# Kernel optimization log

Measured on AMD Instinct MI355X. Metric: run time of the kernel, lower is better.

## Reference

```python
import jax, jax.numpy as jnp
import numpy as np

B, S, D, H, HS = 2, 2048, 1024, 16, 64


def setup_inputs() -> dict:
    key = jax.random.key(0)
    ks = jax.random.split(key, 4)
    x = jax.random.normal(ks[0], (B, S, D), dtype=jnp.float32)
    # causal mask: 1.0 where key_pos <= query_pos, else 0.0
    mask = jnp.tril(jnp.ones((S, S), dtype=jnp.float32))
    w_qkv = jax.random.normal(ks[1], (D, 3, H, HS), dtype=jnp.float32) * 0.02
    b_qkv = jnp.zeros((3, H, HS), dtype=jnp.float32)
    w_proj = jax.random.normal(ks[2], (H, HS, D), dtype=jnp.float32) * 0.02
    b_proj = jnp.zeros((D,), dtype=jnp.float32)
    return {"x": x, "mask": mask, "w_qkv": w_qkv, "b_qkv": b_qkv,
            "w_proj": w_proj, "b_proj": b_proj}


def reference(x, mask, w_qkv, b_qkv, w_proj, b_proj):
    # c_attn: [B,S,D] @ [D,3,H,HS] -> [B,S,3,H,HS]
    qkv = jnp.einsum('bsd,dthc->bsthc', x, w_qkv) + b_qkv
    q, k, v = qkv[:, :, 0], qkv[:, :, 1], qkv[:, :, 2]  # [B,S,H,HS]
    scale = jax.lax.rsqrt(float(HS))
    q = q * scale
    # scores over head_size: [B,H,S(query),S(key)]
    scores = jnp.einsum('bqhc,bkhc->bhqk', q, k)
    scores = scores + (1.0 - mask) * -1e9
    weights = jax.nn.softmax(scores, axis=-1).astype(x.dtype)
    # attn_pdrop = 0.0 / inference: dropout is identity
    attn = jnp.einsum('bhqk,bkhc->bqhc', weights, v)  # [B,S,H,HS]
    out = jnp.einsum('bqhc,hcd->bqd', attn, w_proj) + b_proj
    return out
```

## Files before the change

### kernel.cpp

```cpp
#include <hip/hip_runtime.h>
#include <hip/hip_bf16.h>


#define Bb 2
#define Ss 2048
#define Dd 1024
#define Hh 16
#define HSs 64

typedef __bf16 bf16x8 __attribute__((ext_vector_type(8)));
typedef float  f32x4  __attribute__((ext_vector_type(4)));

__device__ __forceinline__ unsigned short f2bf(float f) {
  unsigned int u = __float_as_uint(f);
  unsigned int lsb = (u >> 16) & 1u;
  u += 0x7fffu + lsb;
  return (unsigned short)(u >> 16);
}

__device__ __forceinline__ void async16(const unsigned short* g, unsigned short* l) {
  __builtin_amdgcn_global_load_lds(
      (const __attribute__((address_space(1))) unsigned int*)g,
      (__attribute__((address_space(3))) unsigned int*)l,
      16, 0, 0);
}

__global__ __launch_bounds__(256) void k_cvt_bf16(const float* __restrict__ in,
                                                  unsigned short* __restrict__ out,
                                                  int n) {
  int i = (blockIdx.x * 256 + threadIdx.x) * 4;
  int stride = gridDim.x * 256 * 4;
  for (; i < n; i += stride) {
    float4 v = *reinterpret_cast<const float4*>(in + i);
    ushort4 o;
    o.x = f2bf(v.x); o.y = f2bf(v.y); o.z = f2bf(v.z); o.w = f2bf(v.w);
    *reinterpret_cast<ushort4*>(out + i) = o;
  }
}

__global__ __launch_bounds__(256) void k_transpose_bf16(const float* __restrict__ in,
                                                        unsigned short* __restrict__ out,
                                                        int R, int C) {
  __shared__ float t[32][33];
  int c0 = blockIdx.x * 32, r0 = blockIdx.y * 32;
  int tx = threadIdx.x, ty = threadIdx.y;
  #pragma unroll
  for (int i = 0; i < 32; i += 8)
    t[ty + i][tx] = in[(size_t)(r0 + ty + i) * C + (c0 + tx)];
  __syncthreads();
  #pragma unroll
  for (int i = 0; i < 32; i += 8)
    out[(size_t)(c0 + ty + i) * R + (r0 + tx)] = f2bf(t[tx][ty + i]);
}

__global__ __launch_bounds__(256) void k_gemm_qkv(const unsigned short* __restrict__ A,
                                                  const unsigned short* __restrict__ Bt,
                                                  const float* __restrict__ bias,
                                                  unsigned short* __restrict__ Qg,
                                                  unsigned short* __restrict__ Kg,
                                                  unsigned short* __restrict__ Vt) {
  __shared__ unsigned short As[128 * 64];
  __shared__ unsigned short Bs[128 * 64];
  const int K = 1024;
  int bid = blockIdx.x;
  int swz = (bid % 8) * 96 + bid / 8;
  int tm = swz / 24, tn = swz % 24;
  int m0 = tm * 128, n0 = tn * 128;
  int tid = threadIdx.x;
  int w = tid >> 6, l = tid & 63;
  int lr = l & 15, lg = l >> 4;
  int wm = (w >> 1) * 64, wn = (w & 1) * 64;
  int srow = l >> 3, scol = (l & 7) * 8;

  f32x4 acc[4][4];
  #pragma unroll
  for (int i = 0; i < 4; ++i)
    #pragma unroll
    for (int j = 0; j < 4; ++j)
      acc[i][j] = (f32x4){0.f, 0.f, 0.f, 0.f};

  for (int k0 = 0; k0 < K; k0 += 64) {
    #pragma unroll
    for (int c = 0; c < 4; ++c) {
      int chunk = w * 4 + c;
      int row = chunk * 8 + srow;
      async16(&A[(size_t)(m0 + row) * K + k0 + scol], &As[chunk * 512]);
      async16(&Bt[(size_t)(n0 + row) * K + k0 + scol], &Bs[chunk * 512]);
    }
    __syncthreads();
    #pragma unroll
    for (int kk = 0; kk < 64; kk += 32) {
      bf16x8 af[4], bfr[4];
      #pragma unroll
      for (int mf = 0; mf < 4; ++mf)
        af[mf] = *reinterpret_cast<const bf16x8*>(&As[(wm + mf * 16 + lr) * 64 + kk + lg * 8]);
      #pragma unroll
      for (int nf = 0; nf < 4; ++nf)
        bfr[nf] = *reinterpret_cast<const bf16x8*>(&Bs[(wn + nf * 16 + lr) * 64 + kk + lg * 8]);
      #pragma unroll
      for (int mf = 0; mf < 4; ++mf)
        #pragma unroll
        for (int nf = 0; nf < 4; ++nf)
          acc[mf][nf] = __builtin_amdgcn_mfma_f32_16x16x32_bf16(af[mf], bfr[nf], acc[mf][nf], 0, 0, 0);
    }
    __syncthreads();
  }

  #pragma unroll
  for (int mf = 0; mf < 4; ++mf) {
    #pragma unroll
    for (int nf = 0; nf < 4; ++nf) {
      int n = n0 + wn + nf * 16 + lr;
      int t = n >> 10, r = n & 1023;
      int h = r >> 6, cc = r & 63;
      float bv = bias[n];
      if (t == 2) {
        int m = m0 + wm + mf * 16 + lg * 4;
        int b = m >> 11, s = m & 2047;
        ushort4 pk;
        pk.x = f2bf(acc[mf][nf][0] + bv);
        pk.y = f2bf(acc[mf][nf][1] + bv);
        pk.z = f2bf(acc[mf][nf][2] + bv);
        pk.w = f2bf(acc[mf][nf][3] + bv);
        *reinterpret_cast<ushort4*>(&Vt[((size_t)(b * Hh + h) * HSs + cc) * Ss + s]) = pk;
      } else {
        #pragma unroll
        for (int j = 0; j < 4; ++j) {
          int m = m0 + wm + mf * 16 + lg * 4 + j;
          int b = m >> 11, s = m & 2047;
          size_t idx = ((size_t)(b * Hh + h) * Ss + s) * HSs + cc;
          float v = acc[mf][nf][j] + bv;
          if (t == 0) Qg[idx] = f2bf(v * 0.1803368801111244f);
          else        Kg[idx] = f2bf(v);
        }
      }
    }
  }
}

__global__ __launch_bounds__(512, 4) void k_attn(const unsigned short* __restrict__ Qg,
                                                 const unsigned short* __restrict__ Kg,
                                                 const unsigned short* __restrict__ Vt,
                                                 unsigned short* __restrict__ Ob) {
  __shared__ unsigned short Ks[2][64 * 64];
  __shared__ unsigned short Vs[2][64 * 64];
  __shared__ unsigned short Ps[8][16 * 72];

  int bid = blockIdx.x;
  int pi = bid >> 5, bh = bid & 31;
  int Q = (pi < 8) ? pi : 23 - pi;
  int b = bh >> 4, h = bh & 15;
  int qs0 = Q * 128;

  int tid = threadIdx.x;
  int w = tid >> 6, l = tid & 63;
  int lr = l & 15, lg = l >> 4;
  int qw = qs0 + w * 16;
  int srow = l >> 3, scol = (l & 7) * 8;
  int swcol = scol ^ (srow << 3);
  int row = w * 8 + srow;

  bf16x8 qf[2];
  #pragma unroll
  for (int kx = 0; kx < 2; ++kx)
    qf[kx] = *reinterpret_cast<const bf16x8*>(
        &Qg[((size_t)bh * Ss + qw + lr) * HSs + kx * 32 + lg * 8]);

  f32x4 oacc[4];
  #pragma unroll
  for (int nf = 0; nf < 4; ++nf) oacc[nf] = (f32x4){0.f, 0.f, 0.f, 0.f};
  float mrun[4], lrun[4];
  #pragma unroll
  for (int j = 0; j < 4; ++j) { mrun[j] = -1e30f; lrun[j] = 0.f; }

  int ntiles = 2 * Q + 2;
  async16(&Kg[((size_t)bh * Ss + row) * HSs + swcol], &Ks[0][w * 512]);
  async16(&Vt[((size_t)bh * HSs + row) * Ss + swcol], &Vs[0][w * 512]);
  __syncthreads();

  for (int t = 0; t < ntiles; ++t) {
    int cur = t & 1;
    if (t + 1 < ntiles) {
      async16(&Kg[((size_t)bh * Ss + (t + 1) * 64 + row) * HSs + swcol], &Ks[cur ^ 1][w * 512]);
      async16(&Vt[((size_t)bh * HSs + row) * Ss + (t + 1) * 64 + swcol], &Vs[cur ^ 1][w * 512]);
    }

    if (t * 64 <= qw + 15) {
      f32x4 sacc[4];
      #pragma unroll
      for (int nf = 0; nf < 4; ++nf) sacc[nf] = (f32x4){0.f, 0.f, 0.f, 0.f};
      __builtin_amdgcn_s_setprio(1);
      #pragma unroll
      for (int kx = 0; kx < 2; ++kx) {
        bf16x8 kf[4];
        #pragma unroll
        for (int nf = 0; nf < 4; ++nf)
          kf[nf] = *reinterpret_cast<const bf16x8*>(
              &Ks[cur][(nf * 16 + lr) * 64 + ((kx * 32 + lg * 8) ^ ((lr & 7) << 3))]);
        #pragma unroll
        for (int nf = 0; nf < 4; ++nf)
          sacc[nf] = __builtin_amdgcn_mfma_f32_16x16x32_bf16(qf[kx], kf[nf], sacc[nf], 0, 0, 0);
      }
      __builtin_amdgcn_s_setprio(0);

      if (t * 64 + 63 > qw) {
        #pragma unroll
        for (int nf = 0; nf < 4; ++nf) {
          int kcol = t * 64 + nf * 16 + lr;
          #pragma unroll
          for (int j = 0; j < 4; ++j) {
            int qg2 = qw + lg * 4 + j;
            if (kcol > qg2) sacc[nf][j] = -1e30f;
          }
        }
      }

      float rmax[4];
      #pragma unroll
      for (int j = 0; j < 4; ++j) {
        float rm = fmaxf(fmaxf(sacc[0][j], sacc[1][j]), fmaxf(sacc[2][j], sacc[3][j]));
        #pragma unroll
        for (int d = 1; d < 16; d <<= 1)
          rm = fmaxf(rm, __shfl_xor(rm, d));
        rmax[j] = rm;
      }
      bool need = (rmax[0] > mrun[0] + 8.f) | (rmax[1] > mrun[1] + 8.f) |
                  (rmax[2] > mrun[2] + 8.f) | (rmax[3] > mrun[3] + 8.f);
      if (__any(need)) {
        #pragma unroll
        for (int j = 0; j < 4; ++j) {
          float mnew = fmaxf(mrun[j], rmax[j]);
          float cf = exp2f(mrun[j] - mnew);
          mrun[j] = mnew;
          lrun[j] *= cf;
          #pragma unroll
          for (int nf = 0; nf < 4; ++nf)
            oacc[nf][j] *= cf;
        }
      }
      #pragma unroll
      for (int j = 0; j < 4; ++j) {
        float psum = 0.f;
        #pragma unroll
        for (int nf = 0; nf < 4; ++nf) {
          float pv = exp2f(sacc[nf][j] - mrun[j]);
          sacc[nf][j] = pv;
          psum += pv;
        }
        #pragma unroll
        for (int d = 1; d < 16; d <<= 1)
          psum += __shfl_xor(psum, d);
        lrun[j] += psum;
      }

      #pragma unroll
      for (int nf = 0; nf < 4; ++nf)
        #pragma unroll
        for (int j = 0; j < 4; ++j)
          Ps[w][(lg * 4 + j) * 72 + nf * 16 + lr] = f2bf(sacc[nf][j]);

      __builtin_amdgcn_s_setprio(1);
      #pragma unroll
      for (int kx = 0; kx < 2; ++kx) {
        bf16x8 pf = *reinterpret_cast<const bf16x8*>(&Ps[w][lr * 72 + kx * 32 + lg * 8]);
        bf16x8 vf[4];
        #pragma unroll
        for (int nf = 0; nf < 4; ++nf)
          vf[nf] = *reinterpret_cast<const bf16x8*>(
              &Vs[cur][(nf * 16 + lr) * 64 + ((kx * 32 + lg * 8) ^ ((lr & 7) << 3))]);
        #pragma unroll
        for (int nf = 0; nf < 4; ++nf)
          oacc[nf] = __builtin_amdgcn_mfma_f32_16x16x32_bf16(pf, vf[nf], oacc[nf], 0, 0, 0);
      }
      __builtin_amdgcn_s_setprio(0);
    }
    __syncthreads();
  }

  #pragma unroll
  for (int j = 0; j < 4; ++j) {
    float rinv = 1.0f / lrun[j];
    int s = qw + lg * 4 + j;
    #pragma unroll
    for (int nf = 0; nf < 4; ++nf) {
      int c = nf * 16 + lr;
      Ob[((size_t)(b * Ss + s)) * Dd + h * HSs + c] = f2bf(oacc[nf][j] * rinv);
    }
  }
}

__global__ __launch_bounds__(256) void k_gemm_out(const unsigned short* __restrict__ A,
                                                  const unsigned short* __restrict__ Bt,
                                                  const float* __restrict__ bias,
                                                  float* __restrict__ Out) {
  __shared__ unsigned short As[128 * 64];
  __shared__ unsigned short Bs[128 * 64];
  const int K = 1024;
  int bid = blockIdx.x;
  int swz = (bid % 8) * 32 + bid / 8;
  int tm = swz / 8, tn = swz % 8;
  int m0 = tm * 128, n0 = tn * 128;
  int tid = threadIdx.x;
  int w = tid >> 6, l = tid & 63;
  int lr = l & 15, lg = l >> 4;
  int wm = (w >> 1) * 64, wn = (w & 1) * 64;
  int srow = l >> 3, scol = (l & 7) * 8;

  f32x4 acc[4][4];
  #pragma unroll
  for (int i = 0; i < 4; ++i)
    #pragma unroll
    for (int j = 0; j < 4; ++j)
      acc[i][j] = (f32x4){0.f, 0.f, 0.f, 0.f};

  for (int k0 = 0; k0 < K; k0 += 64) {
    #pragma unroll
    for (int c = 0; c < 4; ++c) {
      int chunk = w * 4 + c;
      int row = chunk * 8 + srow;
      async16(&A[(size_t)(m0 + row) * K + k0 + scol], &As[chunk * 512]);
      async16(&Bt[(size_t)(n0 + row) * K + k0 + scol], &Bs[chunk * 512]);
    }
    __syncthreads();
    #pragma unroll
    for (int kk = 0; kk < 64; kk += 32) {
      bf16x8 af[4], bfr[4];
      #pragma unroll
      for (int mf = 0; mf < 4; ++mf)
        af[mf] = *reinterpret_cast<const bf16x8*>(&As[(wm + mf * 16 + lr) * 64 + kk + lg * 8]);
      #pragma unroll
      for (int nf = 0; nf < 4; ++nf)
        bfr[nf] = *reinterpret_cast<const bf16x8*>(&Bs[(wn + nf * 16 + lr) * 64 + kk + lg * 8]);
      #pragma unroll
      for (int mf = 0; mf < 4; ++mf)
        #pragma unroll
        for (int nf = 0; nf < 4; ++nf)
          acc[mf][nf] = __builtin_amdgcn_mfma_f32_16x16x32_bf16(af[mf], bfr[nf], acc[mf][nf], 0, 0, 0);
    }
    __syncthreads();
  }

  #pragma unroll
  for (int mf = 0; mf < 4; ++mf)
    #pragma unroll
    for (int nf = 0; nf < 4; ++nf) {
      int n = n0 + wn + nf * 16 + lr;
      float bv = bias[n];
      #pragma unroll
      for (int j = 0; j < 4; ++j) {
        int m = m0 + wm + mf * 16 + lg * 4 + j;
        Out[(size_t)m * 1024 + n] = acc[mf][nf][j] + bv;
      }
    }
}

extern "C" void kernel_launch(void* const* d_in, const int* in_sizes, int n_in,
                              void* d_out, int out_size, void* d_ws, size_t ws_size,
                              hipStream_t stream) {
  (void)in_sizes; (void)n_in; (void)out_size; (void)ws_size;
  const float* x      = (const float*)d_in[0];
  const float* w_qkv  = (const float*)d_in[2];
  const float* b_qkv  = (const float*)d_in[3];
  const float* w_proj = (const float*)d_in[4];
  const float* b_proj = (const float*)d_in[5];
  float* out = (float*)d_out;

  char* ws = (char*)d_ws;
  unsigned short* xb    = (unsigned short*)(ws);
  unsigned short* wqkvT = (unsigned short*)(ws + 8388608);
  unsigned short* wpT   = (unsigned short*)(ws + 14680064);
  unsigned short* Qg    = (unsigned short*)(ws + 16777216);
  unsigned short* Kg    = (unsigned short*)(ws + 25165824);
  unsigned short* Vt    = (unsigned short*)(ws + 33554432);
  unsigned short* attnb = (unsigned short*)(ws + 41943040);

  k_cvt_bf16<<<dim3(2048), dim3(256), 0, stream>>>(x, xb, Bb * Ss * Dd);
  k_transpose_bf16<<<dim3(96, 32), dim3(32, 8), 0, stream>>>(w_qkv, wqkvT, 1024, 3072);
  k_transpose_bf16<<<dim3(32, 32), dim3(32, 8), 0, stream>>>(w_proj, wpT, 1024, 1024);
  k_gemm_qkv<<<dim3(32 * 24), dim3(256), 0, stream>>>(xb, wqkvT, b_qkv, Qg, Kg, Vt);
  k_attn<<<dim3(512), dim3(512), 0, stream>>>(Qg, Kg, Vt, attnb);
  k_gemm_out<<<dim3(32 * 8), dim3(256), 0, stream>>>(attnb, wpT, b_proj, out);
}
```

Measured before the change: 250.8 us.

## Use 128-wide KV tiles in attention and stage V-transpose stores through LDS

The attention kernel now processes 128-key tiles instead of 64-key tiles, which halves the number of loop iterations and barriers per query block. It drops the double-buffered prefetch and per-warp tile skipping, and applies the causal mask only on the diagonal tile. It also remaps blocks so each pair of CTAs covers a query tile and its mirror, balancing causal work. The QKV GEMM epilogue for V now transposes through shared memory so Vt can be written with coalesced 16-byte stores. Losing the prefetch overlap exposes load latency, and warps on the diagonal tile do extra masked work.

```diff
diff --git a/kernel.cpp b/kernel.cpp
--- a/kernel.cpp
+++ b/kernel.cpp
@@ -59,8 +59,7 @@
                                                   unsigned short* __restrict__ Qg,
                                                   unsigned short* __restrict__ Kg,
                                                   unsigned short* __restrict__ Vt) {
-  __shared__ unsigned short As[128 * 64];
-  __shared__ unsigned short Bs[128 * 64];
+  __shared__ unsigned short S[2][128 * 64];
   const int K = 1024;
   int bid = blockIdx.x;
   int swz = (bid % 8) * 96 + bid / 8;
@@ -84,8 +83,8 @@
     for (int c = 0; c < 4; ++c) {
       int chunk = w * 4 + c;
       int row = chunk * 8 + srow;
-      async16(&A[(size_t)(m0 + row) * K + k0 + scol], &As[chunk * 512]);
-      async16(&Bt[(size_t)(n0 + row) * K + k0 + scol], &Bs[chunk * 512]);
+      async16(&A[(size_t)(m0 + row) * K + k0 + scol], &S[0][chunk * 512]);
+      async16(&Bt[(size_t)(n0 + row) * K + k0 + scol], &S[1][chunk * 512]);
     }
     __syncthreads();
     #pragma unroll
@@ -93,10 +92,10 @@
       bf16x8 af[4], bfr[4];
       #pragma unroll
       for (int mf = 0; mf < 4; ++mf)
-        af[mf] = *reinterpret_cast<const bf16x8*>(&As[(wm + mf * 16 + lr) * 64 + kk + lg * 8]);
+        af[mf] = *reinterpret_cast<const bf16x8*>(&S[0][(wm + mf * 16 + lr) * 64 + kk + lg * 8]);
       #pragma unroll
       for (int nf = 0; nf < 4; ++nf)
-        bfr[nf] = *reinterpret_cast<const bf16x8*>(&Bs[(wn + nf * 16 + lr) * 64 + kk + lg * 8]);
+        bfr[nf] = *reinterpret_cast<const bf16x8*>(&S[1][(wn + nf * 16 + lr) * 64 + kk + lg * 8]);
       #pragma unroll
       for (int mf = 0; mf < 4; ++mf)
         #pragma unroll
@@ -106,24 +105,15 @@
     __syncthreads();
   }
 
-  #pragma unroll
-  for (int mf = 0; mf < 4; ++mf) {
-    #pragma unroll
-    for (int nf = 0; nf < 4; ++nf) {
-      int n = n0 + wn + nf * 16 + lr;
-      int t = n >> 10, r = n & 1023;
-      int h = r >> 6, cc = r & 63;
-      float bv = bias[n];
-      if (t == 2) {
-        int m = m0 + wm + mf * 16 + lg * 4;
-        int b = m >> 11, s = m & 2047;
-        ushort4 pk;
-        pk.x = f2bf(acc[mf][nf][0] + bv);
-        pk.y = f2bf(acc[mf][nf][1] + bv);
-        pk.z = f2bf(acc[mf][nf][2] + bv);
-        pk.w = f2bf(acc[mf][nf][3] + bv);
-        *reinterpret_cast<ushort4*>(&Vt[((size_t)(b * Hh + h) * HSs + cc) * Ss + s]) = pk;
-      } else {
+  if (n0 < 2048) {
+    #pragma unroll
+    for (int mf = 0; mf < 4; ++mf) {
+      #pragma unroll
+      for (int nf = 0; nf < 4; ++nf) {
+        int n = n0 + wn + nf * 16 + lr;
+        int t = n >> 10, r = n & 1023;
+        int h = r >> 6, cc = r & 63;
+        float bv = bias[n];
         #pragma unroll
         for (int j = 0; j < 4; ++j) {
           int m = m0 + wm + mf * 16 + lg * 4 + j;
@@ -135,6 +125,32 @@
         }
       }
     }
+  } else {
+    unsigned short* Ts = &S[0][0];
+    #pragma unroll
+    for (int mf = 0; mf < 4; ++mf)
+      #pragma unroll
+      for (int nf = 0; nf < 4; ++nf) {
+        int nl = wn + nf * 16 + lr;
+        float bv = bias[n0 + nl];
+        #pragma unroll
+        for (int j = 0; j < 4; ++j) {
+          int ml = wm + mf * 16 + lg * 4 + j;
+          Ts[nl * 128 + (ml ^ ((nl & 7) << 3))] = f2bf(acc[mf][nf][j] + bv);
+        }
+      }
+    __syncthreads();
+    int nl = tid >> 1, mh = (tid & 1) * 64;
+    int n = n0 + nl;
+    int h = (n & 1023) >> 6, cc = n & 63;
+    int bb = m0 >> 11, s0 = m0 & 2047;
+    unsigned short* dst = &Vt[((size_t)(bb * Hh + h) * HSs + cc) * Ss + s0];
+    #pragma unroll
+    for (int i = 0; i < 8; ++i) {
+      int m = mh + i * 8;
+      bf16x8 v = *reinterpret_cast<const bf16x8*>(&Ts[nl * 128 + (m ^ ((nl & 7) << 3))]);
+      *reinterpret_cast<bf16x8*>(&dst[m]) = v;
+    }
   }
 }
 
@@ -142,23 +158,22 @@
                                                  const unsigned short* __restrict__ Kg,
                                                  const unsigned short* __restrict__ Vt,
                                                  unsigned short* __restrict__ Ob) {
-  __shared__ unsigned short Ks[2][64 * 64];
-  __shared__ unsigned short Vs[2][64 * 64];
-  __shared__ unsigned short Ps[8][16 * 72];
+  __shared__ unsigned short Ks[128 * 64];
+  __shared__ unsigned short Vs[64 * 128];
+  __shared__ unsigned short Ps[8][16 * 128];
 
   int bid = blockIdx.x;
-  int pi = bid >> 5, bh = bid & 31;
-  int Q = (pi < 8) ? pi : 23 - pi;
+  int c = bid >> 8, bh = (bid >> 3) & 31, p = bid & 7;
+  int qt = c ? (15 - p) : p;
   int b = bh >> 4, h = bh & 15;
-  int qs0 = Q * 128;
+  int qs0 = qt * 128;
 
   int tid = threadIdx.x;
   int w = tid >> 6, l = tid & 63;
   int lr = l & 15, lg = l >> 4;
   int qw = qs0 + w * 16;
-  int srow = l >> 3, scol = (l & 7) * 8;
-  int swcol = scol ^ (srow << 3);
-  int row = w * 8 + srow;
+  int srow = l >> 3, scolK = (l & 7) * 8;
+  int rrV = l >> 4, colV = (l & 15) * 8;
 
   bf16x8 qf[2];
   #pragma unroll
@@ -173,106 +188,104 @@
   #pragma unroll
   for (int j = 0; j < 4; ++j) { mrun[j] = -1e30f; lrun[j] = 0.f; }
 
-  int ntiles = 2 * Q + 2;
-  async16(&Kg[((size_t)bh * Ss + row) * HSs + swcol], &Ks[0][w * 512]);
-  async16(&Vt[((size_t)bh * HSs + row) * Ss + swcol], &Vs[0][w * 512]);
-  __syncthreads();
-
+  int ntiles = qt + 1;
   for (int t = 0; t < ntiles; ++t) {
-    int cur = t & 1;
-    if (t + 1 < ntiles) {
-      async16(&Kg[((size_t)bh * Ss + (t + 1) * 64 + row) * HSs + swcol], &Ks[cur ^ 1][w * 512]);
-      async16(&Vt[((size_t)bh * HSs + row) * Ss + (t + 1) * 64 + swcol], &Vs[cur ^ 1][w * 512]);
-    }
-
-    if (t * 64 <= qw + 15) {
-      f32x4 sacc[4];
-      #pragma unroll
-      for (int nf = 0; nf < 4; ++nf) sacc[nf] = (f32x4){0.f, 0.f, 0.f, 0.f};
-      __builtin_amdgcn_s_setprio(1);
-      #pragma unroll
-      for (int kx = 0; kx < 2; ++kx) {
-        bf16x8 kf[4];
+    #pragma unroll
+    for (int cc = 0; cc < 2; ++cc) {
+      int ch = w * 2 + cc;
+      int rowK = ch * 8 + srow;
+      int swK = scolK ^ ((srow & 7) << 3);
+      async16(&Kg[((size_t)bh * Ss + t * 128 + rowK) * HSs + swK], &Ks[ch * 512]);
+      int rowV = ch * 4 + rrV;
+      int swV = colV ^ ((rowV & 7) << 3);
+      async16(&Vt[((size_t)bh * HSs + rowV) * Ss + t * 128 + swV], &Vs[ch * 512]);
+    }
+    __syncthreads();
+
+    f32x4 sacc[8];
+    #pragma unroll
+    for (int nf = 0; nf < 8; ++nf) sacc[nf] = (f32x4){0.f, 0.f, 0.f, 0.f};
+    #pragma unroll
+    for (int kx = 0; kx < 2; ++kx) {
+      #pragma unroll
+      for (int nf = 0; nf < 8; ++nf) {
+        int rk = nf * 16 + lr;
+        bf16x8 kf = *reinterpret_cast<const bf16x8*>(
+            &Ks[rk * 64 + ((kx * 32 + lg * 8) ^ ((rk & 7) << 3))]);
+        sacc[nf] = __builtin_amdgcn_mfma_f32_16x16x32_bf16(qf[kx], kf, sacc[nf], 0, 0, 0);
+      }
+    }
+
+    if (t == qt) {
+      #pragma unroll
+      for (int nf = 0; nf < 8; ++nf) {
+        int kcol = qs0 + nf * 16 + lr;
+        #pragma unroll
+        for (int j = 0; j < 4; ++j) {
+          int qg2 = qw + lg * 4 + j;
+          if (kcol > qg2) sacc[nf][j] = -1e30f;
+        }
+      }
+    }
+
+    float rmax[4];
+    #pragma unroll
+    for (int j = 0; j < 4; ++j) {
+      float rm = fmaxf(fmaxf(fmaxf(sacc[0][j], sacc[1][j]), fmaxf(sacc[2][j], sacc[3][j])),
+                       fmaxf(fmaxf(sacc[4][j], sacc[5][j]), fmaxf(sacc[6][j], sacc[7][j])));
+      #pragma unroll
+      for (int d = 1; d < 16; d <<= 1)
+        rm = fmaxf(rm, __shfl_xor(rm, d));
+      rmax[j] = rm;
+    }
+    bool need = (rmax[0] > mrun[0] + 8.f) | (rmax[1] > mrun[1] + 8.f) |
+                (rmax[2] > mrun[2] + 8.f) | (rmax[3] > mrun[3] + 8.f);
+    if (__any(need)) {
+      #pragma unroll
+      for (int j = 0; j < 4; ++j) {
+        float mnew = fmaxf(mrun[j], rmax[j]);
+        float cf = exp2f(mrun[j] - mnew);
+        mrun[j] = mnew;
+        lrun[j] *= cf;
         #pragma unroll
         for (int nf = 0; nf < 4; ++nf)
-          kf[nf] = *reinterpret_cast<const bf16x8*>(
-              &Ks[cur][(nf * 16 + lr) * 64 + ((kx * 32 + lg * 8) ^ ((lr & 7) << 3))]);
-        #pragma unroll
-        for (int nf = 0; nf < 4; ++nf)
-          sacc[nf] = __builtin_amdgcn_mfma_f32_16x16x32_bf16(qf[kx], kf[nf], sacc[nf], 0, 0, 0);
-      }
-      __builtin_amdgcn_s_setprio(0);
-
-      if (t * 64 + 63 > qw) {
-        #pragma unroll
-        for (int nf = 0; nf < 4; ++nf) {
-          int kcol = t * 64 + nf * 16 + lr;
-          #pragma unroll
-          for (int j = 0; j < 4; ++j) {
-            int qg2 = qw + lg * 4 + j;
-            if (kcol > qg2) sacc[nf][j] = -1e30f;
-          }
-        }
-      }
-
-      float rmax[4];
+          oacc[nf][j] *= cf;
+      }
+    }
+    #pragma unroll
+    for (int j = 0; j < 4; ++j) {
+      float psum = 0.f;
+      #pragma unroll
+      for (int nf = 0; nf < 8; ++nf) {
+        float pv = exp2f(sacc[nf][j] - mrun[j]);
+        sacc[nf][j] = pv;
+        psum += pv;
+      }
+      #pragma unroll
+      for (int d = 1; d < 16; d <<= 1)
+        psum += __shfl_xor(psum, d);
+      lrun[j] += psum;
+    }
+
+    #pragma unroll
+    for (int nf = 0; nf < 8; ++nf)
       #pragma unroll
       for (int j = 0; j < 4; ++j) {
-        float rm = fmaxf(fmaxf(sacc[0][j], sacc[1][j]), fmaxf(sacc[2][j], sacc[3][j]));
-        #pragma unroll
-        for (int d = 1; d < 16; d <<= 1)
-          rm = fmaxf(rm, __shfl_xor(rm, d));
-        rmax[j] = rm;
-      }
-      bool need = (rmax[0] > mrun[0] + 8.f) | (rmax[1] > mrun[1] + 8.f) |
-                  (rmax[2] > mrun[2] + 8.f) | (rmax[3] > mrun[3] + 8.f);
-      if (__any(need)) {
-        #pragma unroll
-        for (int j = 0; j < 4; ++j) {
-          float mnew = fmaxf(mrun[j], rmax[j]);
-          float cf = exp2f(mrun[j] - mnew);
-          mrun[j] = mnew;
-          lrun[j] *= cf;
-          #pragma unroll
-          for (int nf = 0; nf < 4; ++nf)
-            oacc[nf][j] *= cf;
-        }
-      }
-      #pragma unroll
-      for (int j = 0; j < 4; ++j) {
-        float psum = 0.f;
-        #pragma unroll
-        for (int nf = 0; nf < 4; ++nf) {
-          float pv = exp2f(sacc[nf][j] - mrun[j]);
-          sacc[nf][j] = pv;
-          psum += pv;
-        }
-        #pragma unroll
-        for (int d = 1; d < 16; d <<= 1)
-          psum += __shfl_xor(psum, d);
-        lrun[j] += psum;
-      }
-
-      #pragma unroll
-      for (int nf = 0; nf < 4; ++nf)
-        #pragma unroll
-        for (int j = 0; j < 4; ++j)
-          Ps[w][(lg * 4 + j) * 72 + nf * 16 + lr] = f2bf(sacc[nf][j]);
-
-      __builtin_amdgcn_s_setprio(1);
-      #pragma unroll
-      for (int kx = 0; kx < 2; ++kx) {
-        bf16x8 pf = *reinterpret_cast<const bf16x8*>(&Ps[w][lr * 72 + kx * 32 + lg * 8]);
-        bf16x8 vf[4];
-        #pragma unroll
-        for (int nf = 0; nf < 4; ++nf)
-          vf[nf] = *reinterpret_cast<const bf16x8*>(
-              &Vs[cur][(nf * 16 + lr) * 64 + ((kx * 32 + lg * 8) ^ ((lr & 7) << 3))]);
-        #pragma unroll
-        for (int nf = 0; nf < 4; ++nf)
-          oacc[nf] = __builtin_amdgcn_mfma_f32_16x16x32_bf16(pf, vf[nf], oacc[nf], 0, 0, 0);
-      }
-      __builtin_amdgcn_s_setprio(0);
+        int prow = lg * 4 + j;
+        Ps[w][prow * 128 + ((nf * 16 + lr) ^ ((prow & 7) << 3))] = f2bf(sacc[nf][j]);
+      }
+
+    #pragma unroll
+    for (int kx = 0; kx < 4; ++kx) {
+      bf16x8 pf = *reinterpret_cast<const bf16x8*>(
+          &Ps[w][lr * 128 + ((kx * 32 + lg * 8) ^ ((lr & 7) << 3))]);
+      #pragma unroll
+      for (int nf = 0; nf < 4; ++nf) {
+        int rv = nf * 16 + lr;
+        bf16x8 vf = *reinterpret_cast<const bf16x8*>(
+            &Vs[rv * 128 + ((kx * 32 + lg * 8) ^ ((rv & 7) << 3))]);
+        oacc[nf] = __builtin_amdgcn_mfma_f32_16x16x32_bf16(pf, vf, oacc[nf], 0, 0, 0);
+      }
     }
     __syncthreads();
   }
@@ -283,8 +296,8 @@
     int s = qw + lg * 4 + j;
     #pragma unroll
     for (int nf = 0; nf < 4; ++nf) {
-      int c = nf * 16 + lr;
-      Ob[((size_t)(b * Ss + s)) * Dd + h * HSs + c] = f2bf(oacc[nf][j] * rinv);
+      int cc = nf * 16 + lr;
+      Ob[((size_t)(b * Ss + s)) * Dd + h * HSs + cc] = f2bf(oacc[nf][j] * rinv);
     }
   }
 }
```

Result: slower. 259.3 us (+3.4%).
